# Kernel optimization log

Measured on AMD Instinct MI355X. Metric: run time of the kernel, lower is better.

Reference implementation:

```python
import jax, jax.numpy as jnp
import numpy as np

B, S, D, H, NB = 512, 200, 256, 4, 2
DH = D // H
N_ITEMS = 100001  # item_num + 1 (padding idx 0)
EPS = 1e-8


def _ln(x, g, b):
    m = x.mean(-1, keepdims=True)
    v = ((x - m) ** 2).mean(-1, keepdims=True)
    return (x - m) / jnp.sqrt(v + EPS) * g + b


def setup_inputs() -> dict:
    key = jax.random.key(0)
    ks = jax.random.split(key, 20)
    f32 = jnp.float32
    item_emb = jax.random.normal(ks[0], (N_ITEMS, D), f32) * 0.02
    item_emb = item_emb.at[0].set(0.0)  # padding_idx=0
    pos_emb = jax.random.normal(ks[1], (S, D), f32) * 0.02
    inp = {
        'item_emb': item_emb,
        'pos_emb': pos_emb,
        'ln1_g': jnp.ones((NB, D), f32),
        'ln1_b': jnp.zeros((NB, D), f32),
        'in_w': jax.random.normal(ks[2], (NB, 3 * D, D), f32) * 0.02,
        'in_b': jnp.zeros((NB, 3 * D), f32),
        'out_w': jax.random.normal(ks[3], (NB, D, D), f32) * 0.02,
        'out_b': jnp.zeros((NB, D), f32),
        'ln2_g': jnp.ones((NB, D), f32),
        'ln2_b': jnp.zeros((NB, D), f32),
        'c1_w': jax.random.normal(ks[4], (NB, D, D), f32) * 0.02,
        'c1_b': jnp.zeros((NB, D), f32),
        'c2_w': jax.random.normal(ks[5], (NB, D, D), f32) * 0.02,
        'c2_b': jnp.zeros((NB, D), f32),
        'last_g': jnp.ones((D,), f32),
        'last_b': jnp.zeros((D,), f32),
        'user_ids': jax.random.randint(ks[6], (B,), 0, 10000),
        'log_seqs': jax.random.randint(ks[7], (B, S), 0, N_ITEMS),
        'pos_seqs': jax.random.randint(ks[8], (B, S), 0, N_ITEMS),
        'neg_seqs': jax.random.randint(ks[9], (B, S), 0, N_ITEMS),
    }
    return inp


def reference(item_emb, pos_emb, ln1_g, ln1_b, in_w, in_b, out_w, out_b,
              ln2_g, ln2_b, c1_w, c1_b, c2_w, c2_b, last_g, last_b,
              user_ids, log_seqs, pos_seqs, neg_seqs):
    seqs = item_emb[log_seqs] * jnp.asarray(D ** 0.5, item_emb.dtype)
    seqs = seqs + pos_emb[None, :, :]  # positions = arange(S)
    tl_mask = (log_seqs != 0)[..., None].astype(seqs.dtype)  # [B,S,1]
    seqs = seqs * tl_mask
    causal = jnp.tril(jnp.ones((S, S), bool))  # True = attend
    scale = 1.0 / np.sqrt(DH)
    for i in range(NB):
        Q = _ln(seqs, ln1_g[i], ln1_b[i])
        q = (Q @ in_w[i, :D].T + in_b[i, :D]).reshape(B, S, H, DH)
        k = (seqs @ in_w[i, D:2 * D].T + in_b[i, D:2 * D]).reshape(B, S, H, DH)
        v = (seqs @ in_w[i, 2 * D:].T + in_b[i, 2 * D:]).reshape(B, S, H, DH)
        scores = jnp.einsum('bqhd,bkhd->bhqk', q, k) * scale
        scores = jnp.where(causal[None, None], scores, -jnp.inf)
        attn = jax.nn.softmax(scores, axis=-1)
        o = jnp.einsum('bhqk,bkhd->bqhd', attn, v).reshape(B, S, D)
        o = o @ out_w[i].T + out_b[i]
        seqs = Q + o  # residual is on layernormed Q (as in source)
        seqs = _ln(seqs, ln2_g[i], ln2_b[i])
        h1 = jax.nn.relu(seqs @ c1_w[i].T + c1_b[i])
        seqs = (h1 @ c2_w[i].T + c2_b[i] + seqs) * tl_mask
    log_feats = _ln(seqs, last_g, last_b)
    pos_embs = item_emb[pos_seqs]
    neg_embs = item_emb[neg_seqs]
    pos_logits = (log_feats * pos_embs).sum(-1)
    neg_logits = (log_feats * neg_embs).sum(-1)
    return (pos_logits, neg_logits)
```

## Files before the change

kernel.cpp:

```cpp
#include <hip/hip_runtime.h>
#include <math.h>

namespace {

constexpr int kB = 512, kS = 200, kD = 256, kH = 4;
constexpr int kM = kB * kS;
constexpr float kEps = 1e-8f;

typedef short bf16x8 __attribute__((ext_vector_type(8)));
typedef float f32x4 __attribute__((ext_vector_type(4)));

__device__ __forceinline__ float bf2f(unsigned short s) {
  return __uint_as_float(((unsigned)s) << 16);
}
__device__ __forceinline__ unsigned cvtpk(float lo, float hi) {
  unsigned r;
  asm("v_cvt_pk_bf16_f32 %0, %1, %2" : "=v"(r) : "v"(lo), "v"(hi));
  return r;
}
__device__ __forceinline__ void gload16(const void* g, void* l) {
  __builtin_amdgcn_global_load_lds(
      (const __attribute__((address_space(1))) void*)g,
      (__attribute__((address_space(3))) void*)l, 16, 0, 0);
}
__device__ __forceinline__ void vm3() { asm volatile("s_waitcnt vmcnt(3)" ::: "memory"); }
__device__ __forceinline__ void vm0() { asm volatile("s_waitcnt vmcnt(0)" ::: "memory"); }
__device__ __forceinline__ void lk0() { asm volatile("s_waitcnt lgkmcnt(0)" ::: "memory"); }
__device__ __forceinline__ void bar() { asm volatile("s_barrier" ::: "memory"); }

__global__ __launch_bounds__(256) void cvt4_kernel(
    const float* __restrict__ w0, const float* __restrict__ w1,
    const float* __restrict__ w2, const float* __restrict__ w3,
    const float* __restrict__ ln1g,
    unsigned short* __restrict__ o0, unsigned short* __restrict__ o1,
    unsigned short* __restrict__ o2, unsigned short* __restrict__ o3) {
  int blk = blockIdx.x;
  const float* src;
  unsigned short* dst;
  int base;
  bool isin = false;
  if (blk < 384)      { src = w0; dst = o0; base = blk; isin = true; }
  else if (blk < 512) { src = w1; dst = o1; base = blk - 384; }
  else if (blk < 640) { src = w2; dst = o2; base = blk - 512; }
  else                { src = w3; dst = o3; base = blk - 640; }
  int i4 = (base * 256 + threadIdx.x) * 4;
  float4 v = *reinterpret_cast<const float4*>(src + i4);
  if (isin) {
    int layer = (i4 >= 196608) ? 1 : 0;
    int rem = i4 - layer * 196608;
    int n = rem >> 8;
    int k = rem & 255;
    if (n < 256) {
      float4 g = *reinterpret_cast<const float4*>(ln1g + layer * 256 + k);
      v.x *= g.x; v.y *= g.y; v.z *= g.z; v.w *= g.w;
    }
  }
  uint2 o = {cvtpk(v.x, v.y), cvtpk(v.z, v.w)};
  *reinterpret_cast<uint2*>(dst + i4) = o;
}

__global__ __launch_bounds__(64) void s1s2_kernel(
    const float* __restrict__ in_w, const float* __restrict__ in_b,
    const float* __restrict__ ln1g, const float* __restrict__ ln1b,
    float* __restrict__ s1o, float* __restrict__ s2o) {
  int blk = blockIdx.x;
  int layer = blk >> 8, n = blk & 255;
  int k = threadIdx.x * 4;
  float4 w = *reinterpret_cast<const float4*>(in_w + (size_t)layer * 196608 + n * 256 + k);
  float4 g = *reinterpret_cast<const float4*>(ln1g + layer * 256 + k);
  float4 b = *reinterpret_cast<const float4*>(ln1b + layer * 256 + k);
  float a = w.x * g.x + w.y * g.y + w.z * g.z + w.w * g.w;
  float c = w.x * b.x + w.y * b.y + w.z * b.z + w.w * b.w;
#pragma unroll
  for (int o = 32; o >= 1; o >>= 1) { a += __shfl_xor(a, o); c += __shfl_xor(c, o); }
  if (threadIdx.x == 0) {
    s1o[blk] = a;
    s2o[blk] = c + in_b[layer * 768 + n];
  }
}

__global__ __launch_bounds__(64) void embed_kernel(
    const float* __restrict__ item_emb, const float* __restrict__ pos_emb,
    const int* __restrict__ log_seqs, unsigned short* __restrict__ x,
    float2* __restrict__ stats) {
  int bs = blockIdx.x;
  int s = bs % kS;
  int idx = log_seqs[bs];
  float msk = (idx != 0) ? 1.f : 0.f;
  int t = threadIdx.x;
  float4 a = reinterpret_cast<const float4*>(item_emb + (size_t)idx * kD)[t];
  float4 p = reinterpret_cast<const float4*>(pos_emb + (size_t)s * kD)[t];
  float v[4];
  v[0] = (a.x * 16.f + p.x) * msk;
  v[1] = (a.y * 16.f + p.y) * msk;
  v[2] = (a.z * 16.f + p.z) * msk;
  v[3] = (a.w * 16.f + p.w) * msk;
  uint2 r = {cvtpk(v[0], v[1]), cvtpk(v[2], v[3])};
  reinterpret_cast<uint2*>(x + (size_t)bs * kD)[t] = r;
  float sm = v[0] + v[1] + v[2] + v[3];
#pragma unroll
  for (int o = 32; o >= 1; o >>= 1) sm += __shfl_xor(sm, o);
  float mean = sm * (1.f / kD);
  float d0 = v[0] - mean, d1 = v[1] - mean, d2 = v[2] - mean, d3 = v[3] - mean;
  float vs = d0 * d0 + d1 * d1 + d2 * d2 + d3 * d3;
#pragma unroll
  for (int o = 32; o >= 1; o >>= 1) vs += __shfl_xor(vs, o);
  if (t == 0) stats[bs] = {mean, rsqrtf(vs * (1.f / kD) + kEps)};
}

template <int MODE, int LN, int G3>
__global__ __launch_bounds__(512, 4) void gemm2(
    const unsigned short* __restrict__ A, int lda,
    const unsigned short* __restrict__ W,
    const float* __restrict__ bias,
    const unsigned short* __restrict__ R, int ldr,
    const int* __restrict__ logseq,
    const float* __restrict__ lng, const float* __restrict__ lnb,
    const float* __restrict__ qg, const float* __restrict__ qb,
    const float2* __restrict__ statsIn, float2* __restrict__ statsOut,
    const float* __restrict__ s1v, const float* __restrict__ s2v,
    unsigned short* __restrict__ C, int ldc) {
  __shared__ __attribute__((aligned(16))) unsigned short SMEM[24576];
  __shared__ float red1[128][4];
  __shared__ float red2[128][4];
  const int tid = threadIdx.x, lane = tid & 63, wid = tid >> 6;
  int m0, n0;
  if (G3) {
    int g = blockIdx.x / 24, sub = blockIdx.x % 24;
    m0 = (g * 8 + (sub & 7)) * 128;
    n0 = (sub >> 3) * 256;
  } else {
    m0 = blockIdx.x * 128;
    n0 = 0;
  }
  const int wm = wid >> 2, wn = wid & 3;
  const int lrow = lane & 15, kgrp = lane >> 4;
  const int srow = tid >> 2;
  const int sslot = (tid & 3) ^ (srow & 3);
  const unsigned short* gA  = A + (size_t)(m0 + srow) * lda + sslot * 8;
  const unsigned short* gW0 = W + (size_t)(n0 + srow) * kD + sslot * 8;
  const unsigned short* gW1 = gW0 + (size_t)128 * kD;
  const int sa = (kgrp ^ (lrow & 3)) * 8;

#define STAGE(kk, bb)                                              \
  do {                                                             \
    gload16(gA + (kk) * 32, &SMEM[(bb) * 4096 + wid * 512]);       \
    gload16(gW0 + (kk) * 32, &SMEM[8192 + (bb) * 8192 + wid * 512]);\
    gload16(gW1 + (kk) * 32, &SMEM[12288 + (bb) * 8192 + wid * 512]);\
  } while (0)

  f32x4 acc[4][4] = {};
  STAGE(0, 0);
  STAGE(1, 1);
#pragma unroll
  for (int k = 0; k < 8; ++k) {
    if (k < 7) vm3(); else vm0();
    bar();
    const int buf = k & 1;
    bf16x8 af[4], bfr[4];
#pragma unroll
    for (int x = 0; x < 4; ++x) {
      af[x]  = *reinterpret_cast<const bf16x8*>(
          &SMEM[8192 + buf * 8192 + (wn * 64 + x * 16 + lrow) * 32 + sa]);
      bfr[x] = *reinterpret_cast<const bf16x8*>(
          &SMEM[buf * 4096 + (wm * 64 + x * 16 + lrow) * 32 + sa]);
    }
    __builtin_amdgcn_s_setprio(1);
#pragma unroll
    for (int na = 0; na < 4; ++na)
#pragma unroll
      for (int mb = 0; mb < 4; ++mb)
        acc[na][mb] = __builtin_amdgcn_mfma_f32_16x16x32_bf16(
            af[na], bfr[mb], acc[na][mb], 0, 0, 0);
    __builtin_amdgcn_s_setprio(0);
    bar();
    if (k + 2 < 8) STAGE(k + 2, buf);
  }
#undef STAGE
  const bool qpath = (MODE == 4) && (n0 == 0);
  float msk[4];
  float2 st[4];
  if (MODE == 3) {
#pragma unroll
    for (int mb = 0; mb < 4; ++mb)
      msk[mb] = (logseq[m0 + wm * 64 + mb * 16 + lrow] != 0) ? 1.f : 0.f;
  }
  if (MODE == 5 || (MODE == 4 && n0 == 0)) {
#pragma unroll
    for (int mb = 0; mb < 4; ++mb)
      st[mb] = statsIn[m0 + wm * 64 + mb * 16 + lrow];
  }

  auto computeX = [&](int na, int mb, float x[4]) {
    const int gcol = n0 + wn * 64 + na * 16 + kgrp * 4;
    const f32x4 v = acc[na][mb];
    if (MODE == 4 && qpath) {
      float4 t1 = *reinterpret_cast<const float4*>(s1v + gcol);
      float4 t2 = *reinterpret_cast<const float4*>(s2v + gcol);
      const float s1f[4] = {t1.x, t1.y, t1.z, t1.w};
      const float s2f[4] = {t2.x, t2.y, t2.z, t2.w};
#pragma unroll
      for (int r = 0; r < 4; ++r)
        x[r] = st[mb].y * (v[r] - st[mb].x * s1f[r]) + s2f[r];
      return;
    }
    float4 b4 = *reinterpret_cast<const float4*>(bias + gcol);
    const float bx[4] = {b4.x, b4.y, b4.z, b4.w};
    if (MODE == 1) {
#pragma unroll
      for (int r = 0; r < 4; ++r) x[r] = fmaxf(v[r] + bx[r], 0.f);
    } else if (MODE == 4) {
#pragma unroll
      for (int r = 0; r < 4; ++r) x[r] = v[r] + bx[r];
    } else if (MODE == 3) {
      int m = m0 + wm * 64 + mb * 16 + lrow;
      ushort4 rv = *reinterpret_cast<const ushort4*>(R + (size_t)m * ldr + gcol);
      const unsigned short* rs = reinterpret_cast<const unsigned short*>(&rv);
#pragma unroll
      for (int r = 0; r < 4; ++r)
        x[r] = (v[r] + bx[r] + bf2f(rs[r])) * msk[mb];
    } else {
      int m = m0 + wm * 64 + mb * 16 + lrow;
      ushort4 rv = *reinterpret_cast<const ushort4*>(R + (size_t)m * ldr + gcol);
      const unsigned short* rs = reinterpret_cast<const unsigned short*>(&rv);
      float4 t1 = *reinterpret_cast<const float4*>(qg + gcol);
      float4 t2 = *reinterpret_cast<const float4*>(qb + gcol);
      const float g4[4] = {t1.x, t1.y, t1.z, t1.w};
      const float qb4[4] = {t2.x, t2.y, t2.z, t2.w};
#pragma unroll
      for (int r = 0; r < 4; ++r) {
        float q = (bf2f(rs[r]) - st[mb].x) * st[mb].y * g4[r] + qb4[r];
        x[r] = v[r] + bx[r] + q;
      }
    }
  };

  float mean[4], inv[4];
  if (LN) {
    float sA[4] = {0.f, 0.f, 0.f, 0.f}, sB[4] = {0.f, 0.f, 0.f, 0.f};
#pragma unroll
    for (int na = 0; na < 4; ++na)
#pragma unroll
      for (int mb = 0; mb < 4; ++mb) {
        float x[4];
        computeX(na, mb, x);
#pragma unroll
        for (int r = 0; r < 4; ++r) { sA[mb] += x[r]; sB[mb] += x[r] * x[r]; }
      }
#pragma unroll
    for (int mb = 0; mb < 4; ++mb) {
      sA[mb] += __shfl_xor(sA[mb], 16); sA[mb] += __shfl_xor(sA[mb], 32);
      sB[mb] += __shfl_xor(sB[mb], 16); sB[mb] += __shfl_xor(sB[mb], 32);
    }
    if (kgrp == 0) {
#pragma unroll
      for (int mb = 0; mb < 4; ++mb) {
        int rl = wm * 64 + mb * 16 + lrow;
        red1[rl][wn] = sA[mb];
        red2[rl][wn] = sB[mb];
      }
    }
    __syncthreads();
#pragma unroll
    for (int mb = 0; mb < 4; ++mb) {
      int rl = wm * 64 + mb * 16 + lrow;
      float4 p1 = *reinterpret_cast<const float4*>(red1[rl]);
      float4 p2 = *reinterpret_cast<const float4*>(red2[rl]);
      float t1 = p1.x + p1.y + p1.z + p1.w;
      float t2 = p2.x + p2.y + p2.z + p2.w;
      float mu = t1 * (1.f / 256.f);
      float var = t2 * (1.f / 256.f) - mu * mu;
      mean[mb] = mu;
      inv[mb] = rsqrtf(fmaxf(var, 0.f) + kEps);
    }
    if (LN == 3 && wn == 0 && kgrp == 0) {
#pragma unroll
      for (int mb = 0; mb < 4; ++mb)
        statsOut[m0 + wm * 64 + mb * 16 + lrow] = {mean[mb], inv[mb]};
    }
  }
  unsigned short* eb = &SMEM[wid * 3072];
  const int rr = lane >> 2, c8 = (lane & 3) * 8;
#pragma unroll
  for (int hh = 0; hh < 2; ++hh) {
    lk0();
#pragma unroll
    for (int mbl = 0; mbl < 2; ++mbl) {
      int mb = hh * 2 + mbl;
#pragma unroll
      for (int na = 0; na < 4; ++na) {
        float x[4];
        computeX(na, mb, x);
        if (LN == 1) {
          int gcol = n0 + wn * 64 + na * 16 + kgrp * 4;
          float4 g4v = *reinterpret_cast<const float4*>(lng + gcol);
          float4 b4v = *reinterpret_cast<const float4*>(lnb + gcol);
          x[0] = (x[0] - mean[mb]) * inv[mb] * g4v.x + b4v.x;
          x[1] = (x[1] - mean[mb]) * inv[mb] * g4v.y + b4v.y;
          x[2] = (x[2] - mean[mb]) * inv[mb] * g4v.z + b4v.z;
          x[3] = (x[3] - mean[mb]) * inv[mb] * g4v.w + b4v.w;
        }
        uint2 o = {cvtpk(x[0], x[1]), cvtpk(x[2], x[3])};
        *reinterpret_cast<uint2*>(&eb[(mbl * 16 + lrow) * 72 + na * 16 + kgrp * 4]) = o;
      }
    }
    lk0();
#pragma unroll
    for (int rh = 0; rh < 2; ++rh) {
      int row = rh * 16 + rr;
      uint4 d0 = *reinterpret_cast<const uint4*>(&eb[row * 72 + c8]);
      uint4 d1 = *reinterpret_cast<const uint4*>(&eb[row * 72 + 32 + c8]);
      size_t gbase = (size_t)(m0 + wm * 64 + hh * 32 + row) * ldc + (n0 + wn * 64 + c8);
      *reinterpret_cast<uint4*>(C + gbase) = d0;
      *reinterpret_cast<uint4*>(C + gbase + 32) = d1;
    }
  }
}

__global__ __launch_bounds__(256) void attn_mfma(unsigned short* __restrict__ qkv) {
  constexpr int kVS = 234, kQS = 768;
  __shared__ __attribute__((aligned(16))) unsigned short Kl[200 * 72];
  __shared__ __attribute__((aligned(16))) unsigned short Vt[64 * kVS];
  __shared__ __attribute__((aligned(16))) unsigned short Pt[4][16 * 40];
  int b = blockIdx.x >> 2, h = blockIdx.x & 3;
  int tid = threadIdx.x, lane = tid & 63, wid = tid >> 6;
  const unsigned short* kvb = qkv + (size_t)b * kS * kQS + 256 + h * 64;
  for (int i = tid; i < 1600; i += 256) {
    int row = i >> 3, c = i & 7;
    *reinterpret_cast<uint4*>(&Kl[row * 72 + c * 8]) =
        *reinterpret_cast<const uint4*>(kvb + (size_t)row * kQS + c * 8);
  }
  for (int i = tid; i < 3200; i += 256) {
    int row = i >> 4, d0 = (i & 15) * 4;
    ushort4 v = *reinterpret_cast<const ushort4*>(kvb + 256 + (size_t)row * kQS + d0);
    Vt[(d0 + 0) * kVS + row] = v.x;
    Vt[(d0 + 1) * kVS + row] = v.y;
    Vt[(d0 + 2) * kVS + row] = v.z;
    Vt[(d0 + 3) * kVS + row] = v.w;
  }
  for (int i = tid; i < 2048; i += 256) {
    int d = i >> 5, c = i & 31;
    Vt[d * kVS + 200 + c] = 0;
  }
  __syncthreads();

  int qcol = lane & 15, kgrp = lane >> 4;
  const float scale2 = 0.18033688f;
  int packed = (wid < 2) ? (wid == 0 ? 0xF45C : 0xF37B)
                         : (wid == 2 ? 0xF26A : 0x0189);
  for (int ti = 0; ti < 4; ++ti) {
    int t = (packed >> (ti * 4)) & 15;
    if (t == 15) break;
    int qb = t * 16;
    int qrow = qb + qcol;
    int qm = min(qrow, kS - 1);
    const unsigned short* qrp = qkv + (size_t)(b * kS + qm) * kQS + h * 64;
    bf16x8 qf0 = *reinterpret_cast<const bf16x8*>(qrp + kgrp * 8);
    bf16x8 qf1 = *reinterpret_cast<const bf16x8*>(qrp + 32 + kgrp * 8);
    f32x4 accO[4] = {};
    float m_run = -3.0e38f, l_run = 0.f;
    int nc = (qb + 47) >> 5;
    for (int c = 0; c < nc; ++c) {
      int kbase = c * 32;
      f32x4 s0 = {}, s1 = {};
      int kr0 = min(kbase + qcol, kS - 1);
      int kr1 = min(kbase + 16 + qcol, kS - 1);
      const unsigned short* K0 = &Kl[kr0 * 72 + kgrp * 8];
      const unsigned short* K1 = &Kl[kr1 * 72 + kgrp * 8];
      s0 = __builtin_amdgcn_mfma_f32_16x16x32_bf16(*reinterpret_cast<const bf16x8*>(K0), qf0, s0, 0, 0, 0);
      s0 = __builtin_amdgcn_mfma_f32_16x16x32_bf16(*reinterpret_cast<const bf16x8*>(K0 + 32), qf1, s0, 0, 0, 0);
      s1 = __builtin_amdgcn_mfma_f32_16x16x32_bf16(*reinterpret_cast<const bf16x8*>(K1), qf0, s1, 0, 0, 0);
      s1 = __builtin_amdgcn_mfma_f32_16x16x32_bf16(*reinterpret_cast<const bf16x8*>(K1 + 32), qf1, s1, 0, 0, 0);
      float sv[8];
      float cm = -3.0e38f;
#pragma unroll
      for (int r = 0; r < 4; ++r) {
        int key0 = kbase + kgrp * 4 + r;
        int key1 = key0 + 16;
        float x0 = (key0 <= qm) ? s0[r] * scale2 : -3.0e38f;
        float x1 = (key1 <= qm) ? s1[r] * scale2 : -3.0e38f;
        sv[r] = x0; sv[r + 4] = x1;
        cm = fmaxf(cm, fmaxf(x0, x1));
      }
      cm = fmaxf(cm, __shfl_xor(cm, 16));
      cm = fmaxf(cm, __shfl_xor(cm, 32));
      if (!__all(cm - m_run <= 8.f)) {
        float m_new = fmaxf(m_run, cm);
        float sc = exp2f(m_run - m_new);
        l_run *= sc;
#pragma unroll
        for (int nf = 0; nf < 4; ++nf) accO[nf] *= sc;
        m_run = m_new;
      }
      float p[8];
      float psum = 0.f;
#pragma unroll
      for (int r = 0; r < 8; ++r) {
        p[r] = exp2f(sv[r] - m_run);
        psum += p[r];
      }
      l_run += psum;
      uint2 w0 = {cvtpk(p[0], p[1]), cvtpk(p[2], p[3])};
      uint2 w1 = {cvtpk(p[4], p[5]), cvtpk(p[6], p[7])};
      *reinterpret_cast<uint2*>(&Pt[wid][qcol * 40 + kgrp * 4]) = w0;
      *reinterpret_cast<uint2*>(&Pt[wid][qcol * 40 + 16 + kgrp * 4]) = w1;
      bf16x8 pf = *reinterpret_cast<const bf16x8*>(&Pt[wid][qcol * 40 + kgrp * 8]);
#pragma unroll
      for (int nf = 0; nf < 4; ++nf) {
        bf16x8 vf = *reinterpret_cast<const bf16x8*>(
            &Vt[(nf * 16 + qcol) * kVS + kbase + kgrp * 8]);
        accO[nf] = __builtin_amdgcn_mfma_f32_16x16x32_bf16(vf, pf, accO[nf], 0, 0, 0);
      }
    }
    float l_tot = l_run;
    l_tot += __shfl_xor(l_tot, 16);
    l_tot += __shfl_xor(l_tot, 32);
    float inv = 1.f / l_tot;
    if (qrow < kS) {
      unsigned short* op = qkv + (size_t)(b * kS + qrow) * kQS + h * 64;
#pragma unroll
      for (int nf = 0; nf < 4; ++nf) {
        uint2 o4 = {cvtpk(accO[nf][0] * inv, accO[nf][1] * inv),
                    cvtpk(accO[nf][2] * inv, accO[nf][3] * inv)};
        *reinterpret_cast<uint2*>(op + nf * 16 + kgrp * 4) = o4;
      }
    }
  }
}

__global__ __launch_bounds__(64) void logits_kernel(
    const unsigned short* __restrict__ feats, const float* __restrict__ item_emb,
    const int* __restrict__ pos_seqs, const int* __restrict__ neg_seqs,
    float* __restrict__ out) {
  int bs = blockIdx.x;
  int t = threadIdx.x;
  ushort4 f4 = reinterpret_cast<const ushort4*>(feats + (size_t)bs * kD)[t];
  float fx = bf2f(f4.x), fy = bf2f(f4.y), fz = bf2f(f4.z), fw = bf2f(f4.w);
  int pi = pos_seqs[bs], ni = neg_seqs[bs];
  float4 p = reinterpret_cast<const float4*>(item_emb + (size_t)pi * kD)[t];
  float4 n = reinterpret_cast<const float4*>(item_emb + (size_t)ni * kD)[t];
  float dp = fx * p.x + fy * p.y + fz * p.z + fw * p.w;
  float dn = fx * n.x + fy * n.y + fz * n.z + fw * n.w;
#pragma unroll
  for (int o = 32; o >= 1; o >>= 1) {
    dp += __shfl_xor(dp, o);
    dn += __shfl_xor(dn, o);
  }
  if (t == 0) {
    out[bs] = dp;
    out[(size_t)kB * kS + bs] = dn;
  }
}

}

extern "C" void kernel_launch(void* const* d_in, const int* in_sizes, int n_in,
                              void* d_out, int out_size, void* d_ws,
                              size_t ws_size, hipStream_t stream) {
  const float* item_emb = (const float*)d_in[0];
  const float* pos_emb  = (const float*)d_in[1];
  const float* ln1_g = (const float*)d_in[2];
  const float* ln1_b = (const float*)d_in[3];
  const float* in_w  = (const float*)d_in[4];
  const float* in_b  = (const float*)d_in[5];
  const float* out_w = (const float*)d_in[6];
  const float* out_b = (const float*)d_in[7];
  const float* ln2_g = (const float*)d_in[8];
  const float* ln2_b = (const float*)d_in[9];
  const float* c1_w  = (const float*)d_in[10];
  const float* c1_b  = (const float*)d_in[11];
  const float* c2_w  = (const float*)d_in[12];
  const float* c2_b  = (const float*)d_in[13];
  const float* last_g = (const float*)d_in[14];
  const float* last_b = (const float*)d_in[15];
  const int* log_seqs = (const int*)d_in[17];
  const int* pos_seqs = (const int*)d_in[18];
  const int* neg_seqs = (const int*)d_in[19];
  float* out = (float*)d_out;

  size_t unit = (size_t)kM * kD;
  unsigned short* X   = (unsigned short*)d_ws;
  unsigned short* QKV = X + unit;
  unsigned short* inw_bf  = X + 4 * unit;
  unsigned short* outw_bf = inw_bf + 2 * 768 * 256;
  unsigned short* c1w_bf  = outw_bf + 2 * 256 * 256;
  unsigned short* c2w_bf  = c1w_bf + 2 * 256 * 256;
  float2* stats = (float2*)(c2w_bf + 2 * 256 * 256);
  float* s1buf = (float*)(stats + 2 * kM);
  float* s2buf = s1buf + 512;

  cvt4_kernel<<<768, 256, 0, stream>>>(in_w, out_w, c1_w, c2_w, ln1_g,
                                       inw_bf, outw_bf, c1w_bf, c2w_bf);
  s1s2_kernel<<<512, 64, 0, stream>>>(in_w, in_b, ln1_g, ln1_b, s1buf, s2buf);
  embed_kernel<<<kM, 64, 0, stream>>>(item_emb, pos_emb, log_seqs, X, stats);

  dim3 g1(kM / 128, 1);
  for (int l = 0; l < 2; ++l) {
    const unsigned short* iw = inw_bf + (size_t)l * 768 * 256;
    float2* stl = stats + (size_t)l * kM;
    gemm2<4, 0, 1><<<kM / 128 * 3, 512, 0, stream>>>(
        X, 256, iw, in_b + l * 768, nullptr, 0, nullptr,
        nullptr, nullptr, nullptr, nullptr, stl, nullptr,
        s1buf + l * 256, s2buf + l * 256, QKV, 768);
    attn_mfma<<<kB * kH, 256, 0, stream>>>(QKV);
    gemm2<5, 1, 0><<<g1, 512, 0, stream>>>(
        QKV, 768, outw_bf + (size_t)l * kD * kD, out_b + l * kD, X, 256, nullptr,
        ln2_g + l * kD, ln2_b + l * kD, ln1_g + l * kD, ln1_b + l * kD,
        stl, nullptr, nullptr, nullptr, QKV + 256, 768);
    gemm2<1, 0, 0><<<g1, 512, 0, stream>>>(
        QKV + 256, 768, c1w_bf + (size_t)l * kD * kD, c1_b + l * kD, nullptr, 0,
        nullptr, nullptr, nullptr, nullptr, nullptr, nullptr, nullptr,
        nullptr, nullptr, QKV + 512, 768);
    if (l == 0) {
      gemm2<3, 3, 0><<<g1, 512, 0, stream>>>(
          QKV + 512, 768, c2w_bf, c2_b, QKV + 256, 768, log_seqs,
          nullptr, nullptr, nullptr, nullptr, nullptr, stats + kM,
          nullptr, nullptr, X, 256);
    } else {
      gemm2<3, 1, 0><<<g1, 512, 0, stream>>>(
          QKV + 512, 768, c2w_bf + (size_t)kD * kD, c2_b + kD, QKV + 256, 768,
          log_seqs, last_g, last_b, nullptr, nullptr, nullptr, nullptr,
          nullptr, nullptr, X, 256);
    }
  }

  logits_kernel<<<kM, 64, 0, stream>>>(X, item_emb, pos_seqs, neg_seqs, out);
}
```

Before: 721.4 us.

## Fuse logits into final GEMM epilogue and rework attention kernel

The final FFN GEMM gets a new MODE 6 epilogue. It applies the last layernorm, gathers the pos/neg item embeddings and reduces the dot products directly into the output, so the separate logits kernel and the write and re-read of the final features go away. The attention kernel now runs 8 waves per block, each taking up to two query tiles, and uses an XOR-swizzled unpadded K layout in LDS to avoid bank conflicts. Online-softmax max tracking is replaced by a fixed offset of -8 in exp2 space. That removes the rescaling work but relies on attention scores staying within a bounded range to avoid overflow or underflow.

```diff
diff --git a/kernel.cpp b/kernel.cpp
--- a/kernel.cpp
+++ b/kernel.cpp
@@ -119,6 +119,8 @@
     const float* __restrict__ qg, const float* __restrict__ qb,
     const float2* __restrict__ statsIn, float2* __restrict__ statsOut,
     const float* __restrict__ s1v, const float* __restrict__ s2v,
+    const float* __restrict__ iembf, const int* __restrict__ posq,
+    const int* __restrict__ negq, float* __restrict__ outlg,
     unsigned short* __restrict__ C, int ldc) {
   __shared__ __attribute__((aligned(16))) unsigned short SMEM[24576];
   __shared__ float red1[128][4];
@@ -180,7 +182,7 @@
   const bool qpath = (MODE == 4) && (n0 == 0);
   float msk[4];
   float2 st[4];
-  if (MODE == 3) {
+  if (MODE == 3 || MODE == 6) {
 #pragma unroll
     for (int mb = 0; mb < 4; ++mb)
       msk[mb] = (logseq[m0 + wm * 64 + mb * 16 + lrow] != 0) ? 1.f : 0.f;
@@ -212,7 +214,7 @@
     } else if (MODE == 4) {
 #pragma unroll
       for (int r = 0; r < 4; ++r) x[r] = v[r] + bx[r];
-    } else if (MODE == 3) {
+    } else if (MODE == 3 || MODE == 6) {
       int m = m0 + wm * 64 + mb * 16 + lrow;
       ushort4 rv = *reinterpret_cast<const ushort4*>(R + (size_t)m * ldr + gcol);
       const unsigned short* rs = reinterpret_cast<const unsigned short*>(&rv);
@@ -279,6 +281,68 @@
         statsOut[m0 + wm * 64 + mb * 16 + lrow] = {mean[mb], inv[mb]};
     }
   }
+
+  if (MODE == 6) {
+    int pi[4], ni[4];
+#pragma unroll
+    for (int mb = 0; mb < 4; ++mb) {
+      int m = m0 + wm * 64 + mb * 16 + lrow;
+      pi[mb] = posq[m];
+      ni[mb] = negq[m];
+    }
+    float pdm[4] = {0.f, 0.f, 0.f, 0.f}, ndm[4] = {0.f, 0.f, 0.f, 0.f};
+#pragma unroll
+    for (int na = 0; na < 4; ++na) {
+      int gcol = n0 + wn * 64 + na * 16 + kgrp * 4;
+      float4 g4v = *reinterpret_cast<const float4*>(lng + gcol);
+      float4 b4v = *reinterpret_cast<const float4*>(lnb + gcol);
+      const float gg[4] = {g4v.x, g4v.y, g4v.z, g4v.w};
+      const float lb[4] = {b4v.x, b4v.y, b4v.z, b4v.w};
+#pragma unroll
+      for (int mb = 0; mb < 4; ++mb) {
+        float x[4];
+        computeX(na, mb, x);
+        float4 pe = *reinterpret_cast<const float4*>(iembf + (size_t)pi[mb] * 256 + gcol);
+        float4 ne = *reinterpret_cast<const float4*>(iembf + (size_t)ni[mb] * 256 + gcol);
+        const float pef[4] = {pe.x, pe.y, pe.z, pe.w};
+        const float nef[4] = {ne.x, ne.y, ne.z, ne.w};
+#pragma unroll
+        for (int r = 0; r < 4; ++r) {
+          float y = (x[r] - mean[mb]) * inv[mb] * gg[r] + lb[r];
+          pdm[mb] += y * pef[r];
+          ndm[mb] += y * nef[r];
+        }
+      }
+    }
+#pragma unroll
+    for (int mb = 0; mb < 4; ++mb) {
+      pdm[mb] += __shfl_xor(pdm[mb], 16); pdm[mb] += __shfl_xor(pdm[mb], 32);
+      ndm[mb] += __shfl_xor(ndm[mb], 16); ndm[mb] += __shfl_xor(ndm[mb], 32);
+    }
+    __syncthreads();
+    if (kgrp == 0) {
+#pragma unroll
+      for (int mb = 0; mb < 4; ++mb) {
+        int rl = wm * 64 + mb * 16 + lrow;
+        red1[rl][wn] = pdm[mb];
+        red2[rl][wn] = ndm[mb];
+      }
+    }
+    __syncthreads();
+    if (wn == 0 && kgrp == 0) {
+#pragma unroll
+      for (int mb = 0; mb < 4; ++mb) {
+        int rl = wm * 64 + mb * 16 + lrow;
+        float4 p1 = *reinterpret_cast<const float4*>(red1[rl]);
+        float4 p2 = *reinterpret_cast<const float4*>(red2[rl]);
+        int m = m0 + rl;
+        outlg[m] = p1.x + p1.y + p1.z + p1.w;
+        outlg[(size_t)kM + m] = p2.x + p2.y + p2.z + p2.w;
+      }
+    }
+    return;
+  }
+
   unsigned short* eb = &SMEM[wid * 3072];
   const int rr = lane >> 2, c8 = (lane & 3) * 8;
 #pragma unroll
@@ -317,20 +381,20 @@
   }
 }
 
-__global__ __launch_bounds__(256) void attn_mfma(unsigned short* __restrict__ qkv) {
-  constexpr int kVS = 234, kQS = 768;
-  __shared__ __attribute__((aligned(16))) unsigned short Kl[200 * 72];
+__global__ __launch_bounds__(512) void attn_mfma(unsigned short* __restrict__ qkv) {
+  constexpr int kVS = 232, kQS = 768;
+  __shared__ __attribute__((aligned(16))) unsigned short Kl[200 * 64];
   __shared__ __attribute__((aligned(16))) unsigned short Vt[64 * kVS];
-  __shared__ __attribute__((aligned(16))) unsigned short Pt[4][16 * 40];
+  __shared__ __attribute__((aligned(16))) unsigned short Pt[8 * 636];
   int b = blockIdx.x >> 2, h = blockIdx.x & 3;
   int tid = threadIdx.x, lane = tid & 63, wid = tid >> 6;
   const unsigned short* kvb = qkv + (size_t)b * kS * kQS + 256 + h * 64;
-  for (int i = tid; i < 1600; i += 256) {
-    int row = i >> 3, c = i & 7;
-    *reinterpret_cast<uint4*>(&Kl[row * 72 + c * 8]) =
-        *reinterpret_cast<const uint4*>(kvb + (size_t)row * kQS + c * 8);
-  }
-  for (int i = tid; i < 3200; i += 256) {
+  for (int i = tid; i < 1600; i += 512) {
+    int row = i >> 3, slot = i & 7;
+    *reinterpret_cast<uint4*>(&Kl[row * 64 + ((slot ^ (row & 7)) << 3)]) =
+        *reinterpret_cast<const uint4*>(kvb + (size_t)row * kQS + slot * 8);
+  }
+  for (int i = tid; i < 3200; i += 512) {
     int row = i >> 4, d0 = (i & 15) * 4;
     ushort4 v = *reinterpret_cast<const ushort4*>(kvb + 256 + (size_t)row * kQS + d0);
     Vt[(d0 + 0) * kVS + row] = v.x;
@@ -338,7 +402,7 @@
     Vt[(d0 + 2) * kVS + row] = v.z;
     Vt[(d0 + 3) * kVS + row] = v.w;
   }
-  for (int i = tid; i < 2048; i += 256) {
+  for (int i = tid; i < 2048; i += 512) {
     int d = i >> 5, c = i & 31;
     Vt[d * kVS + 200 + c] = 0;
   }
@@ -346,9 +410,10 @@
 
   int qcol = lane & 15, kgrp = lane >> 4;
   const float scale2 = 0.18033688f;
-  int packed = (wid < 2) ? (wid == 0 ? 0xF45C : 0xF37B)
-                         : (wid == 2 ? 0xF26A : 0x0189);
-  for (int ti = 0; ti < 4; ++ti) {
+  int packed = (wid < 3) ? (0xFFFC - wid) : (0xFF09 + (wid - 3) * 15);
+  unsigned short* ptw = &Pt[wid * 636];
+#pragma unroll
+  for (int ti = 0; ti < 2; ++ti) {
     int t = (packed >> (ti * 4)) & 15;
     if (t == 15) break;
     int qb = t * 16;
@@ -358,53 +423,39 @@
     bf16x8 qf0 = *reinterpret_cast<const bf16x8*>(qrp + kgrp * 8);
     bf16x8 qf1 = *reinterpret_cast<const bf16x8*>(qrp + 32 + kgrp * 8);
     f32x4 accO[4] = {};
-    float m_run = -3.0e38f, l_run = 0.f;
+    float l_run = 0.f;
     int nc = (qb + 47) >> 5;
     for (int c = 0; c < nc; ++c) {
       int kbase = c * 32;
       f32x4 s0 = {}, s1 = {};
       int kr0 = min(kbase + qcol, kS - 1);
       int kr1 = min(kbase + 16 + qcol, kS - 1);
-      const unsigned short* K0 = &Kl[kr0 * 72 + kgrp * 8];
-      const unsigned short* K1 = &Kl[kr1 * 72 + kgrp * 8];
-      s0 = __builtin_amdgcn_mfma_f32_16x16x32_bf16(*reinterpret_cast<const bf16x8*>(K0), qf0, s0, 0, 0, 0);
-      s0 = __builtin_amdgcn_mfma_f32_16x16x32_bf16(*reinterpret_cast<const bf16x8*>(K0 + 32), qf1, s0, 0, 0, 0);
-      s1 = __builtin_amdgcn_mfma_f32_16x16x32_bf16(*reinterpret_cast<const bf16x8*>(K1), qf0, s1, 0, 0, 0);
-      s1 = __builtin_amdgcn_mfma_f32_16x16x32_bf16(*reinterpret_cast<const bf16x8*>(K1 + 32), qf1, s1, 0, 0, 0);
-      float sv[8];
-      float cm = -3.0e38f;
+      const unsigned short* K0a = &Kl[kr0 * 64 + ((kgrp ^ (kr0 & 7)) << 3)];
+      const unsigned short* K0b = &Kl[kr0 * 64 + (((kgrp + 4) ^ (kr0 & 7)) << 3)];
+      const unsigned short* K1a = &Kl[kr1 * 64 + ((kgrp ^ (kr1 & 7)) << 3)];
+      const unsigned short* K1b = &Kl[kr1 * 64 + (((kgrp + 4) ^ (kr1 & 7)) << 3)];
+      s0 = __builtin_amdgcn_mfma_f32_16x16x32_bf16(*reinterpret_cast<const bf16x8*>(K0a), qf0, s0, 0, 0, 0);
+      s0 = __builtin_amdgcn_mfma_f32_16x16x32_bf16(*reinterpret_cast<const bf16x8*>(K0b), qf1, s0, 0, 0, 0);
+      s1 = __builtin_amdgcn_mfma_f32_16x16x32_bf16(*reinterpret_cast<const bf16x8*>(K1a), qf0, s1, 0, 0, 0);
+      s1 = __builtin_amdgcn_mfma_f32_16x16x32_bf16(*reinterpret_cast<const bf16x8*>(K1b), qf1, s1, 0, 0, 0);
+      float p[8];
+      float psum = 0.f;
 #pragma unroll
       for (int r = 0; r < 4; ++r) {
         int key0 = kbase + kgrp * 4 + r;
         int key1 = key0 + 16;
-        float x0 = (key0 <= qm) ? s0[r] * scale2 : -3.0e38f;
-        float x1 = (key1 <= qm) ? s1[r] * scale2 : -3.0e38f;
-        sv[r] = x0; sv[r + 4] = x1;
-        cm = fmaxf(cm, fmaxf(x0, x1));
-      }
-      cm = fmaxf(cm, __shfl_xor(cm, 16));
-      cm = fmaxf(cm, __shfl_xor(cm, 32));
-      if (!__all(cm - m_run <= 8.f)) {
-        float m_new = fmaxf(m_run, cm);
-        float sc = exp2f(m_run - m_new);
-        l_run *= sc;
-#pragma unroll
-        for (int nf = 0; nf < 4; ++nf) accO[nf] *= sc;
-        m_run = m_new;
-      }
-      float p[8];
-      float psum = 0.f;
-#pragma unroll
-      for (int r = 0; r < 8; ++r) {
-        p[r] = exp2f(sv[r] - m_run);
-        psum += p[r];
+        float x0 = (key0 <= qm) ? fmaf(s0[r], scale2, -8.f) : -3.0e38f;
+        float x1 = (key1 <= qm) ? fmaf(s1[r], scale2, -8.f) : -3.0e38f;
+        p[r] = exp2f(x0);
+        p[r + 4] = exp2f(x1);
+        psum += p[r] + p[r + 4];
       }
       l_run += psum;
       uint2 w0 = {cvtpk(p[0], p[1]), cvtpk(p[2], p[3])};
       uint2 w1 = {cvtpk(p[4], p[5]), cvtpk(p[6], p[7])};
-      *reinterpret_cast<uint2*>(&Pt[wid][qcol * 40 + kgrp * 4]) = w0;
-      *reinterpret_cast<uint2*>(&Pt[wid][qcol * 40 + 16 + kgrp * 4]) = w1;
-      bf16x8 pf = *reinterpret_cast<const bf16x8*>(&Pt[wid][qcol * 40 + kgrp * 8]);
+      *reinterpret_cast<uint2*>(&ptw[qcol * 40 + kgrp * 4]) = w0;
+      *reinterpret_cast<uint2*>(&ptw[qcol * 40 + 16 + kgrp * 4]) = w1;
+      bf16x8 pf = *reinterpret_cast<const bf16x8*>(&ptw[qcol * 40 + kgrp * 8]);
 #pragma unroll
       for (int nf = 0; nf < 4; ++nf) {
         bf16x8 vf = *reinterpret_cast<const bf16x8*>(
@@ -425,30 +476,6 @@
         *reinterpret_cast<uint2*>(op + nf * 16 + kgrp * 4) = o4;
       }
     }
-  }
-}
-
-__global__ __launch_bounds__(64) void logits_kernel(
-    const unsigned short* __restrict__ feats, const float* __restrict__ item_emb,
-    const int* __restrict__ pos_seqs, const int* __restrict__ neg_seqs,
-    float* __restrict__ out) {
-  int bs = blockIdx.x;
-  int t = threadIdx.x;
-  ushort4 f4 = reinterpret_cast<const ushort4*>(feats + (size_t)bs * kD)[t];
-  float fx = bf2f(f4.x), fy = bf2f(f4.y), fz = bf2f(f4.z), fw = bf2f(f4.w);
-  int pi = pos_seqs[bs], ni = neg_seqs[bs];
-  float4 p = reinterpret_cast<const float4*>(item_emb + (size_t)pi * kD)[t];
-  float4 n = reinterpret_cast<const float4*>(item_emb + (size_t)ni * kD)[t];
-  float dp = fx * p.x + fy * p.y + fz * p.z + fw * p.w;
-  float dn = fx * n.x + fy * n.y + fz * n.z + fw * n.w;
-#pragma unroll
-  for (int o = 32; o >= 1; o >>= 1) {
-    dp += __shfl_xor(dp, o);
-    dn += __shfl_xor(dn, o);
-  }
-  if (t == 0) {
-    out[bs] = dp;
-    out[(size_t)kB * kS + bs] = dn;
   }
 }
 
@@ -501,28 +528,28 @@
     gemm2<4, 0, 1><<<kM / 128 * 3, 512, 0, stream>>>(
         X, 256, iw, in_b + l * 768, nullptr, 0, nullptr,
         nullptr, nullptr, nullptr, nullptr, stl, nullptr,
-        s1buf + l * 256, s2buf + l * 256, QKV, 768);
-    attn_mfma<<<kB * kH, 256, 0, stream>>>(QKV);
+        s1buf + l * 256, s2buf + l * 256, nullptr, nullptr, nullptr, nullptr,
+        QKV, 768);
+    attn_mfma<<<kB * kH, 512, 0, stream>>>(QKV);
     gemm2<5, 1, 0><<<g1, 512, 0, stream>>>(
         QKV, 768, outw_bf + (size_t)l * kD * kD, out_b + l * kD, X, 256, nullptr,
         ln2_g + l * kD, ln2_b + l * kD, ln1_g + l * kD, ln1_b + l * kD,
-        stl, nullptr, nullptr, nullptr, QKV + 256, 768);
+        stl, nullptr, nullptr, nullptr, nullptr, nullptr, nullptr, nullptr,
+        QKV + 256, 768);
     gemm2<1, 0, 0><<<g1, 512, 0, stream>>>(
         QKV + 256, 768, c1w_bf + (size_t)l * kD * kD, c1_b + l * kD, nullptr, 0,
         nullptr, nullptr, nullptr, nullptr, nullptr, nullptr, nullptr,
-        nullptr, nullptr, QKV + 512, 768);
+        nullptr, nullptr, nullptr, nullptr, nullptr, nullptr, QKV + 512, 768);
     if (l == 0) {
       gemm2<3, 3, 0><<<g1, 512, 0, stream>>>(
           QKV + 512, 768, c2w_bf, c2_b, QKV + 256, 768, log_seqs,
           nullptr, nullptr, nullptr, nullptr, nullptr, stats + kM,
-          nullptr, nullptr, X, 256);
+          nullptr, nullptr, nullptr, nullptr, nullptr, nullptr, X, 256);
     } else {
-      gemm2<3, 1, 0><<<g1, 512, 0, stream>>>(
+      gemm2<6, 1, 0><<<g1, 512, 0, stream>>>(
           QKV + 512, 768, c2w_bf + (size_t)kD * kD, c2_b + kD, QKV + 256, 768,
           log_seqs, last_g, last_b, nullptr, nullptr, nullptr, nullptr,
-          nullptr, nullptr, X, 256);
-    }
-  }
-
-  logits_kernel<<<kM, 64, 0, stream>>>(X, item_emb, pos_seqs, neg_seqs, out);
-}
+          nullptr, nullptr, item_emb, pos_seqs, neg_seqs, out, X, 256);
+    }
+  }
+}
```

Measured after the change: 681.3 us. 5.6% less time.
